# Optimization experiments

Hardware: AMD Instinct MI355X
Metric: run time of the kernel (lower is better)

The kernel has to match this reference:

```python
import jax, jax.numpy as jnp
import numpy as np

TOKEN_DIM = 4
EPS = 1e-6


def setup_inputs() -> dict:
    key = jax.random.key(0)
    k_x, k_w = jax.random.split(key)
    B, S, E = 8, 8192, 512
    EMB = 512
    x = jax.random.normal(k_x, (B, S, E), dtype=jnp.float32)
    ln_gamma = jnp.ones((E,), dtype=jnp.float32)
    ln_beta = jnp.zeros((E,), dtype=jnp.float32)
    # glorot-ish scale for the compression kernel [token_dim*E, EMB]
    W = jax.random.normal(k_w, (TOKEN_DIM * E, EMB), dtype=jnp.float32) * 0.02
    b = jnp.zeros((EMB,), dtype=jnp.float32)
    return {"x": x, "ln_gamma": ln_gamma, "ln_beta": ln_beta, "W": W, "b": b}


def reference(x, ln_gamma, ln_beta, W, b):
    B, S, E = x.shape
    # LayerNormalization over the feature axis (center + scale)
    mean = jnp.mean(x, axis=-1, keepdims=True)
    var = jnp.mean(jnp.square(x - mean), axis=-1, keepdims=True)
    h = (x - mean) * jax.lax.rsqrt(var + EPS) * ln_gamma + ln_beta
    # Divide: split sequence axis by token_dim and merge factor into feature axis
    # [B, S, E] -> [B, S//T, T*E]
    h = h.reshape(B, S // TOKEN_DIM, TOKEN_DIM * E)
    # Dense compression + exact gelu (keras 'gelu' uses erf form)
    out = jnp.einsum('bsf,fd->bsd', h, W) + b
    return jax.nn.gelu(out, approximate=False)
```

## Files before the change

### kernel.cpp

```cpp
#include <hip/hip_runtime.h>
#include <hip/hip_bf16.h>
#include <cstdint>

#define XROWS   65536
#define E       512
#define MROWS   16384
#define KDIM    2048
#define NDIM    512
#define NT      32

typedef __attribute__((ext_vector_type(4))) float f32x4;
typedef __attribute__((ext_vector_type(8))) unsigned short u16x8;
typedef __attribute__((ext_vector_type(8))) __bf16 bf16x8;

__device__ __forceinline__ unsigned short f2bf(float f) {
  unsigned u = __builtin_bit_cast(unsigned, f);
  u += 0x7FFFu + ((u >> 16) & 1u);
  return (unsigned short)(u >> 16);
}

typedef const __attribute__((address_space(1))) unsigned char ga_u8;
typedef __attribute__((address_space(3))) unsigned char ls_u8;
__device__ __forceinline__ void gload16(const void* g, void* l) {
  __builtin_amdgcn_global_load_lds((ga_u8*)g, (ls_u8*)l, 16, 0, 0);
}

__device__ __forceinline__ float gelu_f(float v) {
  float p = v * (2.3022083f + 0.1029432f * (v * v));
  p = fminf(p, 80.0f);
  const float Ee = exp2f(p);
  return v * Ee * __builtin_amdgcn_rcpf(Ee + 1.0f);
}

__global__ __launch_bounds__(256) void setup_kernel(const float* __restrict__ W,
                                                    const float* __restrict__ gamma,
                                                    const float* __restrict__ beta,
                                                    unsigned short* __restrict__ WT,
                                                    float* __restrict__ partial) {
  __shared__ float tile[64][68];
  const int t = threadIdx.x;
  if (blockIdx.x >= 256) {
    const int bk = blockIdx.x - 256;
    float a0 = 0.f, a1 = 0.f;
    for (int k = 0; k < 64; ++k) {
      const int kg = bk * 64 + k;
      const float be = beta[kg & (E - 1)];
      a0 += be * W[(size_t)kg * NDIM + t];
      a1 += be * W[(size_t)kg * NDIM + 256 + t];
    }
    partial[bk * NDIM + t] = a0;
    partial[bk * NDIM + 256 + t] = a1;
    return;
  }
  const int bk = blockIdx.x >> 3;
  const int bn = blockIdx.x & 7;
  const int c4 = (t & 15) * 4;
#pragma unroll
  for (int i = 0; i < 4; ++i) {
    const int r = (t >> 4) + i * 16;
    const f32x4 v = *(const f32x4*)&W[(size_t)(bk * 64 + r) * NDIM + bn * 64 + c4];
    tile[r][c4 + 0] = v.x; tile[r][c4 + 1] = v.y;
    tile[r][c4 + 2] = v.z; tile[r][c4 + 3] = v.w;
  }
  __syncthreads();
#pragma unroll
  for (int j = 0; j < 2; ++j) {
    const int n  = j * 32 + (t >> 3);
    const int kb = (t & 7) * 8;
    const int kg0 = (bk & 7) * 64 + kb;
    const f32x4 g0 = *(const f32x4*)(gamma + kg0);
    const f32x4 g1 = *(const f32x4*)(gamma + kg0 + 4);
    const float gg[8] = {g0.x, g0.y, g0.z, g0.w, g1.x, g1.y, g1.z, g1.w};
    u16x8 o;
#pragma unroll
    for (int q = 0; q < 8; ++q) o[q] = f2bf(gg[q] * tile[kb + q][n]);
    *(u16x8*)&WT[(size_t)(bn * 64 + n) * KDIM + bk * 64 + kb] = o;
  }
}

__global__ __launch_bounds__(256) void kbias2(const float* __restrict__ b,
                                              const float* __restrict__ partial,
                                              float* __restrict__ biasf) {
  const int c = blockIdx.x * 256 + threadIdx.x;
  float s = b[c];
  for (int j = 0; j < 32; ++j) s += partial[j * NDIM + c];
  biasf[c] = s;
}

__global__ __launch_bounds__(256, 4) void ln_kernel(const float* __restrict__ x,
                                                    unsigned short* __restrict__ h) {
  const int w = threadIdx.x >> 6, l = threadIdx.x & 63;
  const size_t row = (size_t)blockIdx.x * 8 + w * 2;
  const float* xr = x + row * E + l * 8;
  const f32x4 a0 = *(const f32x4*)xr;
  const f32x4 a1 = *(const f32x4*)(xr + 4);
  const f32x4 b0 = *(const f32x4*)(xr + E);
  const f32x4 b1 = *(const f32x4*)(xr + E + 4);
  float av[8] = {a0.x, a0.y, a0.z, a0.w, a1.x, a1.y, a1.z, a1.w};
  float bv[8] = {b0.x, b0.y, b0.z, b0.w, b1.x, b1.y, b1.z, b1.w};
  float s0 = 0.f, q0 = 0.f, s1 = 0.f, q1 = 0.f;
#pragma unroll
  for (int j = 0; j < 8; ++j) {
    s0 += av[j]; q0 += av[j] * av[j];
    s1 += bv[j]; q1 += bv[j] * bv[j];
  }
#pragma unroll
  for (int off = 32; off > 0; off >>= 1) {
    s0 += __shfl_xor(s0, off); q0 += __shfl_xor(q0, off);
    s1 += __shfl_xor(s1, off); q1 += __shfl_xor(q1, off);
  }
  const float mean0 = s0 * (1.0f / E);
  const float rstd0 = rsqrtf(q0 * (1.0f / E) - mean0 * mean0 + 1e-6f);
  const float nm0   = -mean0 * rstd0;
  const float mean1 = s1 * (1.0f / E);
  const float rstd1 = rsqrtf(q1 * (1.0f / E) - mean1 * mean1 + 1e-6f);
  const float nm1   = -mean1 * rstd1;
  u16x8 o0, o1;
#pragma unroll
  for (int j = 0; j < 8; ++j) {
    o0[j] = f2bf(av[j] * rstd0 + nm0);
    o1[j] = f2bf(bv[j] * rstd1 + nm1);
  }
  *(u16x8*)(h + row * E + l * 8) = o0;
  *(u16x8*)(h + (row + 1) * E + l * 8) = o1;
}

__global__ __launch_bounds__(256, 3) void gemm_kernel(const unsigned short* __restrict__ A,
                                                      const unsigned short* __restrict__ Bt,
                                                      const float* __restrict__ biasf,
                                                      float* __restrict__ out) {
  __shared__ char smem[32768];
  const int tid = threadIdx.x;
  const int l = tid & 63, w = tid >> 6;
  const int l7 = l & 7, l15 = l & 15, lhi = l >> 4;
  const int wr = w >> 1, wc = w & 1;

  const int wg = ((blockIdx.x & 7) << 6) | (blockIdx.x >> 3);
  const int bn = wg & 3;
  const int bm = wg >> 2;
  const size_t arow0 = (size_t)bm * 128;
  const int    brow0 = bn * 128;

  const int srow = w * 8 + (l >> 3);
  const int swz  = (l7 * 16) ^ ((l >> 3) << 4);
  const char* gA = (const char*)A  + ((size_t)(arow0 + srow) * KDIM) * 2 + swz;
  const char* gB = (const char*)Bt + ((size_t)(brow0 + srow) * KDIM) * 2 + swz;

  f32x4 acc[4][4];
#pragma unroll
  for (int m = 0; m < 4; ++m)
#pragma unroll
    for (int n = 0; n < 4; ++n) acc[m][n] = (f32x4){0.f, 0.f, 0.f, 0.f};

  const int cs0 = (lhi * 16) ^ (l7 * 16);

  for (int t = 0; t < NT; ++t) {
    __syncthreads();
    {
      const char* pa = gA + (size_t)t * 128;
      const char* pb = gB + (size_t)t * 128;
#pragma unroll
      for (int i = 0; i < 4; ++i) {
        gload16(pa + (size_t)i * 32 * KDIM * 2, smem + (i * 32 + w * 8) * 128);
        gload16(pb + (size_t)i * 32 * KDIM * 2, smem + 16384 + (i * 32 + w * 8) * 128);
      }
    }
    __syncthreads();
#pragma unroll
    for (int kk = 0; kk < 2; ++kk) {
      const int co = cs0 ^ (kk * 64);
      bf16x8 av[4], bv[4];
#pragma unroll
      for (int m = 0; m < 4; ++m)
        av[m] = *(const bf16x8*)(smem + (wr * 64 + m * 16 + l15) * 128 + co);
#pragma unroll
      for (int n = 0; n < 4; ++n)
        bv[n] = *(const bf16x8*)(smem + 16384 + (wc * 64 + n * 16 + l15) * 128 + co);
#pragma unroll
      for (int m = 0; m < 4; ++m)
#pragma unroll
        for (int n = 0; n < 4; ++n)
          acc[m][n] = __builtin_amdgcn_mfma_f32_16x16x32_bf16(av[m], bv[n],
                                                              acc[m][n], 0, 0, 0);
    }
  }

#pragma unroll
  for (int n = 0; n < 4; ++n) {
    const int col = brow0 + wc * 64 + n * 16 + l15;
    const float bb = biasf[col];
#pragma unroll
    for (int m = 0; m < 4; ++m) {
      const size_t rbase = arow0 + wr * 64 + m * 16 + lhi * 4;
#pragma unroll
      for (int r = 0; r < 4; ++r) {
        const float v = acc[m][n][r] + bb;
        out[(rbase + r) * NDIM + col] = gelu_f(v);
      }
    }
  }
}

extern "C" void kernel_launch(void* const* d_in, const int* in_sizes, int n_in,
                              void* d_out, int out_size, void* d_ws, size_t ws_size,
                              hipStream_t stream) {
  const float* x     = (const float*)d_in[0];
  const float* gamma = (const float*)d_in[1];
  const float* beta  = (const float*)d_in[2];
  const float* W     = (const float*)d_in[3];
  const float* b     = (const float*)d_in[4];
  float* out = (float*)d_out;

  char* p = (char*)d_ws;
  unsigned short* WT = (unsigned short*)p;            p += (size_t)NDIM * KDIM * 2;
  unsigned short* h  = (unsigned short*)p;            p += (size_t)MROWS * KDIM * 2;
  float* partial     = (float*)p;                     p += (size_t)32 * NDIM * 4;
  float* biasf       = (float*)p;

  setup_kernel<<<288, 256, 0, stream>>>(W, gamma, beta, WT, partial);
  kbias2<<<2, 256, 0, stream>>>(b, partial, biasf);
  ln_kernel<<<XROWS / 8, 256, 0, stream>>>(x, h);
  gemm_kernel<<<(MROWS / 128) * 4, 256, 0, stream>>>(h, WT, biasf, out);
}
```

Baseline: 79.98 us.

## Fuse LayerNorm normalization into GEMM A-tile loads using precomputed row stats

The LN kernel now only computes per-row rstd and -mean*rstd. The GEMM reads raw fp32 x directly into LDS, then normalizes and converts it to bf16 while building the MFMA operands. This drops the bf16 h intermediate write and re-read. In exchange, x is read twice (stats pass plus GEMM) in fp32 by each of the 4 column blocks, LDS use grows to 52KB, and the normalize and convert arithmetic moves into the GEMM inner loop.

```diff
diff --git a/kernel.cpp b/kernel.cpp
--- a/kernel.cpp
+++ b/kernel.cpp
@@ -10,6 +10,7 @@
 #define NT      32
 
 typedef __attribute__((ext_vector_type(4))) float f32x4;
+typedef __attribute__((ext_vector_type(2))) float f32x2;
 typedef __attribute__((ext_vector_type(8))) unsigned short u16x8;
 typedef __attribute__((ext_vector_type(8))) __bf16 bf16x8;
 
@@ -87,8 +88,8 @@
   biasf[c] = s;
 }
 
-__global__ __launch_bounds__(256, 4) void ln_kernel(const float* __restrict__ x,
-                                                    unsigned short* __restrict__ h) {
+__global__ __launch_bounds__(256, 4) void stats_kernel(const float* __restrict__ x,
+                                                       f32x2* __restrict__ stats) {
   const int w = threadIdx.x >> 6, l = threadIdx.x & 63;
   const size_t row = (size_t)blockIdx.x * 8 + w * 2;
   const float* xr = x + row * E + l * 8;
@@ -109,27 +110,24 @@
     s0 += __shfl_xor(s0, off); q0 += __shfl_xor(q0, off);
     s1 += __shfl_xor(s1, off); q1 += __shfl_xor(q1, off);
   }
-  const float mean0 = s0 * (1.0f / E);
-  const float rstd0 = rsqrtf(q0 * (1.0f / E) - mean0 * mean0 + 1e-6f);
-  const float nm0   = -mean0 * rstd0;
-  const float mean1 = s1 * (1.0f / E);
-  const float rstd1 = rsqrtf(q1 * (1.0f / E) - mean1 * mean1 + 1e-6f);
-  const float nm1   = -mean1 * rstd1;
-  u16x8 o0, o1;
-#pragma unroll
-  for (int j = 0; j < 8; ++j) {
-    o0[j] = f2bf(av[j] * rstd0 + nm0);
-    o1[j] = f2bf(bv[j] * rstd1 + nm1);
-  }
-  *(u16x8*)(h + row * E + l * 8) = o0;
-  *(u16x8*)(h + (row + 1) * E + l * 8) = o1;
-}
-
-__global__ __launch_bounds__(256, 3) void gemm_kernel(const unsigned short* __restrict__ A,
+  if (l == 0) {
+    const float m0 = s0 * (1.0f / E);
+    const float r0 = rsqrtf(q0 * (1.0f / E) - m0 * m0 + 1e-6f);
+    const float m1 = s1 * (1.0f / E);
+    const float r1 = rsqrtf(q1 * (1.0f / E) - m1 * m1 + 1e-6f);
+    f32x2 o0; o0.x = r0; o0.y = -m0 * r0;
+    f32x2 o1; o1.x = r1; o1.y = -m1 * r1;
+    stats[row] = o0;
+    stats[row + 1] = o1;
+  }
+}
+
+__global__ __launch_bounds__(256, 3) void gemm_kernel(const float* __restrict__ x,
+                                                      const f32x2* __restrict__ stats,
                                                       const unsigned short* __restrict__ Bt,
                                                       const float* __restrict__ biasf,
                                                       float* __restrict__ out) {
-  __shared__ char smem[32768];
+  __shared__ char smem[53248];
   const int tid = threadIdx.x;
   const int l = tid & 63, w = tid >> 6;
   const int l7 = l & 7, l15 = l & 15, lhi = l >> 4;
@@ -141,10 +139,12 @@
   const size_t arow0 = (size_t)bm * 128;
   const int    brow0 = bn * 128;
 
+  const int r7 = (tid >> 4) & 7;
+  const char* gX = (const char*)x + ((size_t)(arow0 + (tid >> 4)) * KDIM) * 4
+                 + (((tid & 15) * 16) ^ (r7 << 5));
   const int srow = w * 8 + (l >> 3);
-  const int swz  = (l7 * 16) ^ ((l >> 3) << 4);
-  const char* gA = (const char*)A  + ((size_t)(arow0 + srow) * KDIM) * 2 + swz;
-  const char* gB = (const char*)Bt + ((size_t)(brow0 + srow) * KDIM) * 2 + swz;
+  const int swzB = (l7 * 16) ^ ((l >> 3) << 4);
+  const char* gB = (const char*)Bt + ((size_t)(brow0 + srow) * KDIM) * 2 + swzB;
 
   f32x4 acc[4][4];
 #pragma unroll
@@ -153,34 +153,55 @@
     for (int n = 0; n < 4; ++n) acc[m][n] = (f32x4){0.f, 0.f, 0.f, 0.f};
 
   const int cs0 = (lhi * 16) ^ (l7 * 16);
+
+  gload16((const char*)stats + arow0 * 32 + tid * 16, smem + 49152 + tid * 16);
 
   for (int t = 0; t < NT; ++t) {
     __syncthreads();
     {
-      const char* pa = gA + (size_t)t * 128;
+      const char* px = gX + (size_t)t * 256;
+#pragma unroll
+      for (int i = 0; i < 8; ++i)
+        gload16(px + (size_t)i * 16 * KDIM * 4, smem + i * 4096 + tid * 16);
       const char* pb = gB + (size_t)t * 128;
 #pragma unroll
-      for (int i = 0; i < 4; ++i) {
-        gload16(pa + (size_t)i * 32 * KDIM * 2, smem + (i * 32 + w * 8) * 128);
-        gload16(pb + (size_t)i * 32 * KDIM * 2, smem + 16384 + (i * 32 + w * 8) * 128);
+      for (int i = 0; i < 4; ++i)
+        gload16(pb + (size_t)i * 32 * KDIM * 2, smem + 32768 + (i * 32 + w * 8) * 128);
+    }
+    __syncthreads();
+
+    const int tok = t >> 3;
+    f32x2 st[4];
+#pragma unroll
+    for (int m = 0; m < 4; ++m)
+      st[m] = *(const f32x2*)(smem + 49152 +
+                              ((wr * 64 + m * 16 + l15) * 4 + tok) * 8);
+#pragma unroll
+    for (int kk = 0; kk < 2; ++kk) {
+      const int coa = (kk * 128 + lhi * 32) ^ (l7 << 5);
+      const int cob = cs0 ^ (kk * 64);
+      bf16x8 avv[4], bv[4];
+#pragma unroll
+      for (int m = 0; m < 4; ++m) {
+        const char* ap = smem + (wr * 64 + m * 16 + l15) * 256 + coa;
+        const f32x4 lo = *(const f32x4*)ap;
+        const f32x4 hi = *(const f32x4*)(ap + 16);
+        const float rs = st[m].x, nm = st[m].y;
+        u16x8 o;
+        o[0] = f2bf(lo.x * rs + nm); o[1] = f2bf(lo.y * rs + nm);
+        o[2] = f2bf(lo.z * rs + nm); o[3] = f2bf(lo.w * rs + nm);
+        o[4] = f2bf(hi.x * rs + nm); o[5] = f2bf(hi.y * rs + nm);
+        o[6] = f2bf(hi.z * rs + nm); o[7] = f2bf(hi.w * rs + nm);
+        avv[m] = __builtin_bit_cast(bf16x8, o);
       }
-    }
-    __syncthreads();
-#pragma unroll
-    for (int kk = 0; kk < 2; ++kk) {
-      const int co = cs0 ^ (kk * 64);
-      bf16x8 av[4], bv[4];
+#pragma unroll
+      for (int n = 0; n < 4; ++n)
+        bv[n] = *(const bf16x8*)(smem + 32768 + (wc * 64 + n * 16 + l15) * 128 + cob);
 #pragma unroll
       for (int m = 0; m < 4; ++m)
-        av[m] = *(const bf16x8*)(smem + (wr * 64 + m * 16 + l15) * 128 + co);
-#pragma unroll
-      for (int n = 0; n < 4; ++n)
-        bv[n] = *(const bf16x8*)(smem + 16384 + (wc * 64 + n * 16 + l15) * 128 + co);
-#pragma unroll
-      for (int m = 0; m < 4; ++m)
 #pragma unroll
         for (int n = 0; n < 4; ++n)
-          acc[m][n] = __builtin_amdgcn_mfma_f32_16x16x32_bf16(av[m], bv[n],
+          acc[m][n] = __builtin_amdgcn_mfma_f32_16x16x32_bf16(avv[m], bv[n],
                                                               acc[m][n], 0, 0, 0);
     }
   }
@@ -213,12 +234,12 @@
 
   char* p = (char*)d_ws;
   unsigned short* WT = (unsigned short*)p;            p += (size_t)NDIM * KDIM * 2;
-  unsigned short* h  = (unsigned short*)p;            p += (size_t)MROWS * KDIM * 2;
+  f32x2* stats       = (f32x2*)p;                     p += (size_t)XROWS * 8;
   float* partial     = (float*)p;                     p += (size_t)32 * NDIM * 4;
   float* biasf       = (float*)p;
 
   setup_kernel<<<288, 256, 0, stream>>>(W, gamma, beta, WT, partial);
   kbias2<<<2, 256, 0, stream>>>(b, partial, biasf);
-  ln_kernel<<<XROWS / 8, 256, 0, stream>>>(x, h);
-  gemm_kernel<<<(MROWS / 128) * 4, 256, 0, stream>>>(h, WT, biasf, out);
-}
+  stats_kernel<<<XROWS / 8, 256, 0, stream>>>(x, stats);
+  gemm_kernel<<<(MROWS / 128) * 4, 256, 0, stream>>>(x, stats, WT, biasf, out);
+}
```

Result: slower. 101.2 us (+26.6%).

## Load GEMM B operand directly into registers with double-buffered prefetch

Applied to the files above, without the earlier changes.

The GEMM no longer stages the B (weight) tile through LDS. Each wave loads its B fragments straight from global memory into registers, double-buffered across even and odd k-steps so the next step's loads overlap the current MFMAs. This halves shared memory and removes the B LDS reads, but raises register use, so launch bounds drop from 3 to 2 blocks per CU. The global B loads are strided per lane and are duplicated across the two row-waves, and the two barriers per k-step remain.

```diff
diff --git a/kernel.cpp b/kernel.cpp
--- a/kernel.cpp
+++ b/kernel.cpp
@@ -125,11 +125,11 @@
   *(u16x8*)(h + (row + 1) * E + l * 8) = o1;
 }
 
-__global__ __launch_bounds__(256, 3) void gemm_kernel(const unsigned short* __restrict__ A,
+__global__ __launch_bounds__(256, 2) void gemm_kernel(const unsigned short* __restrict__ A,
                                                       const unsigned short* __restrict__ Bt,
                                                       const float* __restrict__ biasf,
                                                       float* __restrict__ out) {
-  __shared__ char smem[32768];
+  __shared__ char smem[16384];
   const int tid = threadIdx.x;
   const int l = tid & 63, w = tid >> 6;
   const int l7 = l & 7, l15 = l & 15, lhi = l >> 4;
@@ -143,8 +143,9 @@
 
   const int srow = w * 8 + (l >> 3);
   const int swz  = (l7 * 16) ^ ((l >> 3) << 4);
-  const char* gA = (const char*)A  + ((size_t)(arow0 + srow) * KDIM) * 2 + swz;
-  const char* gB = (const char*)Bt + ((size_t)(brow0 + srow) * KDIM) * 2 + swz;
+  const char* gA = (const char*)A + ((size_t)(arow0 + srow) * KDIM) * 2 + swz;
+
+  const unsigned short* gBF = Bt + (size_t)(brow0 + wc * 64 + l15) * KDIM + lhi * 8;
 
   f32x4 acc[4][4];
 #pragma unroll
@@ -154,36 +155,57 @@
 
   const int cs0 = (lhi * 16) ^ (l7 * 16);
 
-  for (int t = 0; t < NT; ++t) {
-    __syncthreads();
-    {
-      const char* pa = gA + (size_t)t * 128;
-      const char* pb = gB + (size_t)t * 128;
-#pragma unroll
-      for (int i = 0; i < 4; ++i) {
-        gload16(pa + (size_t)i * 32 * KDIM * 2, smem + (i * 32 + w * 8) * 128);
-        gload16(pb + (size_t)i * 32 * KDIM * 2, smem + 16384 + (i * 32 + w * 8) * 128);
-      }
-    }
-    __syncthreads();
-#pragma unroll
-    for (int kk = 0; kk < 2; ++kk) {
-      const int co = cs0 ^ (kk * 64);
-      bf16x8 av[4], bv[4];
-#pragma unroll
-      for (int m = 0; m < 4; ++m)
-        av[m] = *(const bf16x8*)(smem + (wr * 64 + m * 16 + l15) * 128 + co);
-#pragma unroll
-      for (int n = 0; n < 4; ++n)
-        bv[n] = *(const bf16x8*)(smem + 16384 + (wc * 64 + n * 16 + l15) * 128 + co);
-#pragma unroll
-      for (int m = 0; m < 4; ++m)
-#pragma unroll
-        for (int n = 0; n < 4; ++n)
-          acc[m][n] = __builtin_amdgcn_mfma_f32_16x16x32_bf16(av[m], bv[n],
-                                                              acc[m][n], 0, 0, 0);
-    }
-  }
+  bf16x8 bvE[8], bvO[8];
+
+#define LOADBV(BV, t)                                                          \
+  _Pragma("unroll")                                                            \
+  for (int kk = 0; kk < 2; ++kk)                                               \
+    _Pragma("unroll")                                                          \
+    for (int n = 0; n < 4; ++n)                                                \
+      BV[kk * 4 + n] = *(const bf16x8*)(gBF + (size_t)n * 16 * KDIM +          \
+                                        (t) * 64 + kk * 32)
+
+#define STAGEA(t)                                                              \
+  {                                                                            \
+    const char* pa = gA + (size_t)(t) * 128;                                   \
+    _Pragma("unroll")                                                          \
+    for (int i = 0; i < 4; ++i)                                                \
+      gload16(pa + (size_t)i * 32 * KDIM * 2, smem + (i * 32 + w * 8) * 128);  \
+  }
+
+#define COMPUTE(BV)                                                            \
+  _Pragma("unroll")                                                            \
+  for (int kk = 0; kk < 2; ++kk) {                                             \
+    const int co = cs0 ^ (kk * 64);                                            \
+    bf16x8 av[4];                                                              \
+    _Pragma("unroll")                                                          \
+    for (int m = 0; m < 4; ++m)                                                \
+      av[m] = *(const bf16x8*)(smem + (wr * 64 + m * 16 + l15) * 128 + co);    \
+    _Pragma("unroll")                                                          \
+    for (int m = 0; m < 4; ++m)                                                \
+      _Pragma("unroll")                                                        \
+      for (int n = 0; n < 4; ++n)                                              \
+        acc[m][n] = __builtin_amdgcn_mfma_f32_16x16x32_bf16(av[m],             \
+                        BV[kk * 4 + n], acc[m][n], 0, 0, 0);                   \
+  }
+
+  LOADBV(bvE, 0);
+
+  for (int t = 0; t < NT; t += 2) {
+    __syncthreads();
+    STAGEA(t);
+    __syncthreads();
+    if (t + 1 < NT) LOADBV(bvO, t + 1);
+    COMPUTE(bvE);
+    __syncthreads();
+    STAGEA(t + 1);
+    __syncthreads();
+    if (t + 2 < NT) LOADBV(bvE, t + 2);
+    COMPUTE(bvO);
+  }
+#undef LOADBV
+#undef STAGEA
+#undef COMPUTE
 
 #pragma unroll
   for (int n = 0; n < 4; ++n) {
```

New measurement: 116.6 us. 1.46x slower.
